# Performance work log

Measured on AMD Instinct MI355X. Metric: run time of the kernel, lower is better.

The kernel has to match this reference:

```python
import jax, jax.numpy as jnp
import numpy as np

N, K, F, H, C = 16384, 16, 3, 64, 10


def setup_inputs() -> dict:
    key = jax.random.key(0)
    ks = jax.random.split(key, 6)
    pos = jax.random.normal(ks[0], (N, F), jnp.float32)
    batch = jnp.zeros((N,), jnp.int32)  # single graph
    W1 = jax.random.normal(ks[1], (2 * F, H), jnp.float32) * 0.1
    b1 = jnp.zeros((H,), jnp.float32)
    W2 = jax.random.normal(ks[2], (2 * H, H), jnp.float32) * 0.1
    b2 = jnp.zeros((H,), jnp.float32)
    Wc = jax.random.normal(ks[3], (H, C), jnp.float32) * 0.1
    bc = jnp.zeros((C,), jnp.float32)
    return {"pos": pos, "batch": batch, "W1": W1, "b1": b1,
            "W2": W2, "b2": b2, "Wc": Wc, "bc": bc}


def knn_graph(pos, k):
    # brute-force knn with self-loops (loop=True): self has distance 0
    sq = jnp.sum(pos * pos, axis=1)
    d = sq[:, None] + sq[None, :] - 2.0 * (pos @ pos.T)  # [N, N]
    _, idx = jax.lax.top_k(-d, k)  # [N, k] nearest neighbor indices (incl. self)
    return idx


def edge_conv(x, idx, W, b):
    # message for edge j->i: Linear(concat(x_i, x_j - x_i)); aggregate by max over neighbors
    n, k = idx.shape
    xi = x[:, None, :]               # [N, 1, F]
    xj = x[idx]                      # [N, k, F]
    msg = jnp.concatenate([jnp.broadcast_to(xi, (n, k, x.shape[1])), xj - xi], axis=-1)
    m = msg @ W + b                  # [N, k, H]
    return jnp.max(m, axis=1)        # [N, H]


def reference(pos, batch, W1, b1, W2, b2, Wc, bc):
    idx = knn_graph(pos, K)
    h = jax.nn.relu(edge_conv(pos, idx, W1, b1))
    h = jax.nn.relu(edge_conv(h, idx, W2, b2))
    g = jax.ops.segment_max(h, batch, num_segments=1)  # global max pool -> [1, H]
    return g @ Wc + bc
```

## Files before the change

kernel.cpp:

```cpp
#include <hip/hip_runtime.h>

#define NPTS 16384
#define KNN 16
#define HID 64
#define NCLS 10

#define WPB 4
#define QPB 16
#define CPW (NPTS / WPB)
#define SCAP 128

__device__ __forceinline__ float distm2(float qx, float qy, float qz, float4 c) {
    return fmaf(qx, c.x, fmaf(qy, c.y, fmaf(qz, c.z, c.w)));
}

__device__ __forceinline__ float __frfl(float x) {
    return __int_as_float(__builtin_amdgcn_readfirstlane(__float_as_int(x)));
}

__device__ __forceinline__ unsigned long long dkey(float v, int j) {
    unsigned u = __float_as_uint(v);
    u = (u & 0x80000000u) ? ~u : (u | 0x80000000u);
    return ((unsigned long long)u << 32) | (unsigned)j;
}

__device__ __forceinline__ unsigned long long shfl_xor_u64(unsigned long long x, int m) {
    unsigned hi = (unsigned)__shfl_xor((int)(x >> 32), m, 64);
    unsigned lo = (unsigned)__shfl_xor((int)(x & 0xffffffffu), m, 64);
    return ((unsigned long long)hi << 32) | lo;
}

__device__ __forceinline__ void wave_top16_16(unsigned long long (&key)[16], int lane,
                                              int q, int* __restrict__ idx) {
    int outj = 0x7fffffff;
    for (int r = 0; r < 16; ++r) {
        unsigned long long gm = key[0];
#pragma unroll
        for (int s = 1; s < 16; ++s) gm = key[s] < gm ? key[s] : gm;
#pragma unroll
        for (int st = 1; st < 64; st <<= 1) {
            unsigned long long o = shfl_xor_u64(gm, st);
            gm = o < gm ? o : gm;
        }
        if (lane == r) outj = (int)(gm & 0xffffffffu);
#pragma unroll
        for (int s = 0; s < 16; ++s)
            if (key[s] == gm) key[s] = ~0ull;
    }
    if (lane < 16) idx[q * KNN + lane] = outj;
}

__global__ void prep_kernel(const float* __restrict__ pos, float4* __restrict__ pos4,
                            float4* __restrict__ pm2) {
    int i = blockIdx.x * 256 + threadIdx.x;
    if (i < NPTS) {
        float x = pos[3 * i], y = pos[3 * i + 1], z = pos[3 * i + 2];
        float sq = fmaf(x, x, fmaf(y, y, z * z));
        pos4[i] = make_float4(x, y, z, sq);
        pm2[i] = make_float4(-2.f * x, -2.f * y, -2.f * z, sq);
    }
}

__global__ __launch_bounds__(256) void knn_kernel(const float4* __restrict__ pos4,
                                                  const float4* __restrict__ pm2,
                                                  int* __restrict__ idx) {
    __shared__ unsigned long long keys[QPB][SCAP];
    __shared__ int knt[QPB];
    __shared__ float smin[QPB][WPB][16];
    int tid = threadIdx.x;
    int lane = tid & 63;
    int w = tid >> 6;
    int qb = blockIdx.x * QPB;
    float qx[QPB], qy[QPB], qz[QPB];
#pragma unroll
    for (int i = 0; i < QPB; ++i) {
        float4 t4 = pos4[qb + i];
        qx[i] = __frfl(t4.x); qy[i] = __frfl(t4.y); qz[i] = __frfl(t4.z);
    }
    int base = w * CPW;

    float mn[QPB];
#pragma unroll
    for (int i = 0; i < QPB; ++i) mn[i] = INFINITY;
    {
        float4 c0 = pm2[base + lane],       c1 = pm2[base + 64 + lane];
        float4 d0 = pm2[base + 128 + lane], d1 = pm2[base + 192 + lane];
        for (int cb = base; cb < base + CPW; cb += 128) {
#pragma unroll
            for (int i = 0; i < QPB; ++i) {
                float va = distm2(qx[i], qy[i], qz[i], c0);
                float vb = distm2(qx[i], qy[i], qz[i], c1);
                mn[i] = fminf(mn[i], fminf(va, vb));
            }
            c0 = d0; c1 = d1;
            d0 = pm2[cb + 256 + lane];
            d1 = pm2[cb + 320 + lane];
        }
    }
#pragma unroll
    for (int i = 0; i < QPB; ++i) {
        float m = mn[i];
        m = fminf(m, __shfl_xor(m, 16, 64));
        m = fminf(m, __shfl_xor(m, 32, 64));
        if (lane < 16) smin[i][w][lane] = m;
    }
    if (tid < QPB) knt[tid] = 0;
    __syncthreads();

    float tq[QPB];
#pragma unroll
    for (int i = 0; i < QPB; ++i) {
        int s = lane & 15;
        float m = fminf(fminf(smin[i][0][s], smin[i][1][s]),
                        fminf(smin[i][2][s], smin[i][3][s]));
        m = fmaxf(m, __shfl_xor(m, 1, 64));
        m = fmaxf(m, __shfl_xor(m, 2, 64));
        m = fmaxf(m, __shfl_xor(m, 4, 64));
        m = fmaxf(m, __shfl_xor(m, 8, 64));
        tq[i] = __frfl(m);
    }

    {
        float4 c0 = pm2[base + lane],       c1 = pm2[base + 64 + lane];
        float4 d0 = pm2[base + 128 + lane], d1 = pm2[base + 192 + lane];
        for (int cb = base; cb < base + CPW; cb += 128) {
            int j0 = cb + lane, j1 = cb + 64 + lane;
#pragma unroll
            for (int i = 0; i < QPB; ++i) {
                float va = distm2(qx[i], qy[i], qz[i], c0);
                float vb = distm2(qx[i], qy[i], qz[i], c1);
                if (fminf(va, vb) <= tq[i]) {
                    if (va <= tq[i]) { int s = atomicAdd(&knt[i], 1); if (s < SCAP) keys[i][s] = dkey(va, j0); }
                    if (vb <= tq[i]) { int s = atomicAdd(&knt[i], 1); if (s < SCAP) keys[i][s] = dkey(vb, j1); }
                }
            }
            c0 = d0; c1 = d1;
            d0 = pm2[cb + 256 + lane];
            d1 = pm2[cb + 320 + lane];
        }
    }
    __syncthreads();

#pragma unroll
    for (int e = 0; e < 4; ++e) {
        int qi = w * 4 + e;
        int q = qb + qi;
        int ntot = knt[qi];
        if (ntot <= SCAP) {
            unsigned long long k0 = (lane < ntot) ? keys[qi][lane] : ~0ull;
            unsigned long long k1 = (lane + 64 < ntot) ? keys[qi][lane + 64] : ~0ull;
            int r0 = 0, r1 = 0;
            int t = 0;
            for (; t + 8 <= ntot; t += 8) {
                unsigned long long a0 = keys[qi][t + 0], a1 = keys[qi][t + 1];
                unsigned long long a2 = keys[qi][t + 2], a3 = keys[qi][t + 3];
                unsigned long long a4 = keys[qi][t + 4], a5 = keys[qi][t + 5];
                unsigned long long a6 = keys[qi][t + 6], a7 = keys[qi][t + 7];
                r0 += (int)(a0 < k0) + (int)(a1 < k0) + (int)(a2 < k0) + (int)(a3 < k0)
                    + (int)(a4 < k0) + (int)(a5 < k0) + (int)(a6 < k0) + (int)(a7 < k0);
                r1 += (int)(a0 < k1) + (int)(a1 < k1) + (int)(a2 < k1) + (int)(a3 < k1)
                    + (int)(a4 < k1) + (int)(a5 < k1) + (int)(a6 < k1) + (int)(a7 < k1);
            }
            for (; t < ntot; ++t) {
                unsigned long long k = keys[qi][t];
                r0 += (int)(k < k0);
                r1 += (int)(k < k1);
            }
            if (lane < ntot && r0 < KNN) idx[q * KNN + r0] = (int)(k0 & 0xffffffffu);
            if (lane + 64 < ntot && r1 < KNN) idx[q * KNN + r1] = (int)(k1 & 0xffffffffu);
        } else {
            float tqq = tq[qi];
            unsigned long long key[16];
#pragma unroll
            for (int u = 0; u < 16; ++u) key[u] = ~0ull;
            for (int j = lane; j < NPTS; j += 64) {
                float v = distm2(qx[qi], qy[qi], qz[qi], pm2[j]);
                unsigned long long k = dkey(v, j);
                if (v <= tqq && k < key[15]) {
#pragma unroll
                    for (int s = 0; s < 16; ++s) {
                        unsigned long long a = k < key[s] ? k : key[s];
                        unsigned long long b = k < key[s] ? key[s] : k;
                        key[s] = a;
                        k = b;
                    }
                }
            }
            wave_top16_16(key, lane, q, idx);
        }
    }
}

__global__ __launch_bounds__(256) void ec12_kernel(const float4* __restrict__ pos4,
                                                   const int* __restrict__ idx,
                                                   const float* __restrict__ W1,
                                                   const float* __restrict__ b1,
                                                   const float* __restrict__ W2,
                                                   const float* __restrict__ b2,
                                                   float* __restrict__ C2,
                                                   float* __restrict__ Y2) {
    __shared__ float h1s[16][64];
    int t = threadIdx.x & 63;
    int w = threadIdx.x >> 6;
    int pb = blockIdx.x * 16 + w * 4;
    float w0 = W1[0 * HID + t], w1 = W1[1 * HID + t], w2 = W1[2 * HID + t];
    float v0 = W1[3 * HID + t], v1 = W1[4 * HID + t], v2 = W1[5 * HID + t];
    float bt1 = b1[t];
#pragma unroll
    for (int i = 0; i < 4; ++i) {
        int p = pb + i;
        float4 xi = pos4[p];
        float C = bt1 + xi.x * (w0 - v0) + xi.y * (w1 - v1) + xi.z * (w2 - v2);
        const int4* ip = (const int4*)(idx + (size_t)p * KNN);
        int4 n0 = ip[0], n1 = ip[1], n2 = ip[2], n3 = ip[3];
        int jj[16] = {n0.x, n0.y, n0.z, n0.w, n1.x, n1.y, n1.z, n1.w,
                      n2.x, n2.y, n2.z, n2.w, n3.x, n3.y, n3.z, n3.w};
        float m = -INFINITY;
#pragma unroll
        for (int k = 0; k < KNN; ++k) {
            float4 xj = pos4[jj[k]];
            m = fmaxf(m, fmaf(xj.x, v0, fmaf(xj.y, v1, xj.z * v2)));
        }
        h1s[w * 4 + i][t] = fmaxf(C + m, 0.f);
    }
    __syncthreads();
    float aa[4] = {0.f, 0.f, 0.f, 0.f};
    float ab[4] = {0.f, 0.f, 0.f, 0.f};
#pragma unroll 8
    for (int f = 0; f < 64; ++f) {
        float wa = W2[f * HID + t];
        float wb = W2[(64 + f) * HID + t];
#pragma unroll
        for (int i = 0; i < 4; ++i) {
            float h = h1s[w * 4 + i][f];
            aa[i] = fmaf(h, wa, aa[i]);
            ab[i] = fmaf(h, wb, ab[i]);
        }
    }
    float bt = b2[t];
#pragma unroll
    for (int i = 0; i < 4; ++i) {
        C2[(pb + i) * HID + t] = bt + aa[i] - ab[i];
        Y2[(pb + i) * HID + t] = ab[i];
    }
}

__global__ __launch_bounds__(256) void ec2_maxpool_kernel(const float* __restrict__ C2,
                                                          const float* __restrict__ Y2,
                                                          const int* __restrict__ idx,
                                                          float* __restrict__ gpartial) {
    int t = threadIdx.x & 63;
    int lp = threadIdx.x >> 6;
    int p = blockIdx.x * 4 + lp;
    const int4* ip = (const int4*)(idx + (size_t)p * KNN);
    int4 n0 = ip[0], n1 = ip[1], n2 = ip[2], n3 = ip[3];
    int jj[16] = {n0.x, n0.y, n0.z, n0.w, n1.x, n1.y, n1.z, n1.w,
                  n2.x, n2.y, n2.z, n2.w, n3.x, n3.y, n3.z, n3.w};
    float m = -INFINITY;
#pragma unroll
    for (int k = 0; k < KNN; ++k) {
        m = fmaxf(m, Y2[jj[k] * HID + t]);
    }
    float val = fmaxf(C2[p * HID + t] + m, 0.f);
    __shared__ float red[4][64];
    red[lp][t] = val;
    __syncthreads();
    if (lp == 0) {
        float g = fmaxf(fmaxf(red[0][t], red[1][t]), fmaxf(red[2][t], red[3][t]));
        gpartial[blockIdx.x * 64 + t] = g;
    }
}

__global__ __launch_bounds__(256) void greduce2_kernel(const float* __restrict__ gpartial,
                                                       float* __restrict__ gp2) {
    __shared__ float red[4][64];
    int f = threadIdx.x & 63;
    int w = threadIdx.x >> 6;
    int r0 = blockIdx.x * 16 + w * 4;
    float m = -INFINITY;
#pragma unroll
    for (int r = 0; r < 4; ++r) m = fmaxf(m, gpartial[(r0 + r) * 64 + f]);
    red[w][f] = m;
    __syncthreads();
    if (w == 0)
        gp2[blockIdx.x * 64 + f] =
            fmaxf(fmaxf(red[0][f], red[1][f]), fmaxf(red[2][f], red[3][f]));
}

__global__ __launch_bounds__(256) void tail2_kernel(const float* __restrict__ gp2,
                                                    const float* __restrict__ Wc,
                                                    const float* __restrict__ bc,
                                                    float* __restrict__ out) {
    __shared__ float red[4][64];
    __shared__ float g[64];
    int f = threadIdx.x & 63;
    int w = threadIdx.x >> 6;
    float m = -INFINITY;
    for (int i = w; i < 256; i += 4) m = fmaxf(m, gp2[i * 64 + f]);
    red[w][f] = m;
    __syncthreads();
    if (w == 0) g[f] = fmaxf(fmaxf(red[0][f], red[1][f]), fmaxf(red[2][f], red[3][f]));
    __syncthreads();
    if (threadIdx.x < NCLS) {
        float a = bc[threadIdx.x];
#pragma unroll
        for (int h = 0; h < HID; ++h) a = fmaf(g[h], Wc[h * NCLS + threadIdx.x], a);
        out[threadIdx.x] = a;
    }
}

extern "C" void kernel_launch(void* const* d_in, const int* in_sizes, int n_in,
                              void* d_out, int out_size, void* d_ws, size_t ws_size,
                              hipStream_t stream) {
    const float* pos = (const float*)d_in[0];
    const float* W1 = (const float*)d_in[2];
    const float* b1 = (const float*)d_in[3];
    const float* W2 = (const float*)d_in[4];
    const float* b2 = (const float*)d_in[5];
    const float* Wc = (const float*)d_in[6];
    const float* bc = (const float*)d_in[7];
    float* out = (float*)d_out;

    char* ws = (char*)d_ws;
    size_t o = 0;
    auto alloc = [&](size_t bytes) { size_t r = o; o += (bytes + 255) & ~size_t(255); return r; };
    size_t fm = (size_t)NPTS * HID * 4;
    size_t o_pos4 = alloc((size_t)NPTS * 16);
    size_t o_pm2 = alloc((size_t)(NPTS + 320) * 16);
    size_t o_idx = alloc((size_t)NPTS * KNN * 4);
    size_t o_C2 = alloc(fm);
    size_t o_Y2 = alloc(fm);
    size_t o_gp = alloc((size_t)(NPTS / 4) * HID * 4);
    size_t o_gp2 = alloc((size_t)256 * HID * 4);

    float4* pos4 = (float4*)(ws + o_pos4);
    float4* pm2 = (float4*)(ws + o_pm2);
    int* idx = (int*)(ws + o_idx);
    float* C2 = (float*)(ws + o_C2);
    float* Y2 = (float*)(ws + o_Y2);
    float* gp = (float*)(ws + o_gp);
    float* gp2 = (float*)(ws + o_gp2);

    hipMemsetAsync(pm2 + NPTS, 0, 320 * sizeof(float4), stream);

    prep_kernel<<<NPTS / 256, 256, 0, stream>>>(pos, pos4, pm2);
    knn_kernel<<<NPTS / QPB, 256, 0, stream>>>(pos4, pm2, idx);
    ec12_kernel<<<NPTS / 16, 256, 0, stream>>>(pos4, idx, W1, b1, W2, b2, C2, Y2);
    ec2_maxpool_kernel<<<NPTS / 4, 256, 0, stream>>>(C2, Y2, idx, gp);
    greduce2_kernel<<<256, 256, 0, stream>>>(gp, gp2);
    tail2_kernel<<<1, 256, 0, stream>>>(gp2, Wc, bc, out);
}
```

Measured before the change: 315.6 us.

## Use packed-FP32 distance math with a paired SoA candidate layout in kNN

```diff
diff --git a/kernel.cpp b/kernel.cpp
--- a/kernel.cpp
+++ b/kernel.cpp
@@ -6,9 +6,19 @@
 #define NCLS 10
 
 #define WPB 4
-#define QPB 16
-#define CPW (NPTS / WPB)
+#define QPB 8
 #define SCAP 128
+#define GRPQ 32
+#define NITER 16
+#define TPAD 576
+
+typedef float v2f __attribute__((ext_vector_type(2)));
+
+__device__ __forceinline__ v2f pdist(v2f Qx, v2f Qy, v2f Qz, v2f X, v2f Y, v2f Z, v2f W) {
+    return __builtin_elementwise_fma(Qx, X,
+            __builtin_elementwise_fma(Qy, Y,
+             __builtin_elementwise_fma(Qz, Z, W)));
+}
 
 __device__ __forceinline__ float distm2(float qx, float qy, float qz, float4 c) {
     return fmaf(qx, c.x, fmaf(qy, c.y, fmaf(qz, c.z, c.w)));
@@ -51,7 +61,7 @@
 }
 
 __global__ void prep_kernel(const float* __restrict__ pos, float4* __restrict__ pos4,
-                            float4* __restrict__ pm2) {
+                            float4* __restrict__ pm2, float4* __restrict__ pm2t) {
     int i = blockIdx.x * 256 + threadIdx.x;
     if (i < NPTS) {
         float x = pos[3 * i], y = pos[3 * i + 1], z = pos[3 * i + 2];
@@ -59,10 +69,21 @@
         pos4[i] = make_float4(x, y, z, sq);
         pm2[i] = make_float4(-2.f * x, -2.f * y, -2.f * z, sq);
     }
+    if (i < NPTS / 2) {
+        int p = i;
+        float x0 = pos[6 * p],     y0 = pos[6 * p + 1], z0 = pos[6 * p + 2];
+        float x1 = pos[6 * p + 3], y1 = pos[6 * p + 4], z1 = pos[6 * p + 5];
+        float w0 = fmaf(x0, x0, fmaf(y0, y0, z0 * z0));
+        float w1 = fmaf(x1, x1, fmaf(y1, y1, z1 * z1));
+        int g = p >> 6, l = p & 63;
+        pm2t[g * 128 + l]      = make_float4(-2.f * x0, -2.f * x1, -2.f * y0, -2.f * y1);
+        pm2t[g * 128 + 64 + l] = make_float4(-2.f * z0, -2.f * z1, w0, w1);
+    }
 }
 
 __global__ __launch_bounds__(256) void knn_kernel(const float4* __restrict__ pos4,
                                                   const float4* __restrict__ pm2,
+                                                  const float4* __restrict__ pm2t,
                                                   int* __restrict__ idx) {
     __shared__ unsigned long long keys[QPB][SCAP];
     __shared__ int knt[QPB];
@@ -71,30 +92,38 @@
     int lane = tid & 63;
     int w = tid >> 6;
     int qb = blockIdx.x * QPB;
-    float qx[QPB], qy[QPB], qz[QPB];
+    v2f Qx[QPB], Qy[QPB], Qz[QPB];
 #pragma unroll
     for (int i = 0; i < QPB; ++i) {
         float4 t4 = pos4[qb + i];
-        qx[i] = __frfl(t4.x); qy[i] = __frfl(t4.y); qz[i] = __frfl(t4.z);
-    }
-    int base = w * CPW;
+        float ax = __frfl(t4.x), ay = __frfl(t4.y), az = __frfl(t4.z);
+        Qx[i] = (v2f){ax, ax}; Qy[i] = (v2f){ay, ay}; Qz[i] = (v2f){az, az};
+    }
+    const float4* pt = pm2t + (size_t)w * (GRPQ * 128) + lane;
 
     float mn[QPB];
 #pragma unroll
     for (int i = 0; i < QPB; ++i) mn[i] = INFINITY;
     {
-        float4 c0 = pm2[base + lane],       c1 = pm2[base + 64 + lane];
-        float4 d0 = pm2[base + 128 + lane], d1 = pm2[base + 192 + lane];
-        for (int cb = base; cb < base + CPW; cb += 128) {
+        float4 aXY0 = pt[0],   aZW0 = pt[64],  aXY1 = pt[128], aZW1 = pt[192];
+        float4 bXY0 = pt[256], bZW0 = pt[320], bXY1 = pt[384], bZW1 = pt[448];
+        int off = 512;
+#pragma unroll 2
+        for (int t = 0; t < NITER; ++t) {
+            v2f X0 = {aXY0.x, aXY0.y}, Y0 = {aXY0.z, aXY0.w};
+            v2f Z0 = {aZW0.x, aZW0.y}, W0 = {aZW0.z, aZW0.w};
+            v2f X1 = {aXY1.x, aXY1.y}, Y1 = {aXY1.z, aXY1.w};
+            v2f Z1 = {aZW1.x, aZW1.y}, W1 = {aZW1.z, aZW1.w};
 #pragma unroll
             for (int i = 0; i < QPB; ++i) {
-                float va = distm2(qx[i], qy[i], qz[i], c0);
-                float vb = distm2(qx[i], qy[i], qz[i], c1);
-                mn[i] = fminf(mn[i], fminf(va, vb));
-            }
-            c0 = d0; c1 = d1;
-            d0 = pm2[cb + 256 + lane];
-            d1 = pm2[cb + 320 + lane];
+                v2f D0 = pdist(Qx[i], Qy[i], Qz[i], X0, Y0, Z0, W0);
+                v2f D1 = pdist(Qx[i], Qy[i], Qz[i], X1, Y1, Z1, W1);
+                mn[i] = fminf(mn[i], fminf(D0.x, D0.y));
+                mn[i] = fminf(mn[i], fminf(D1.x, D1.y));
+            }
+            aXY0 = bXY0; aZW0 = bZW0; aXY1 = bXY1; aZW1 = bZW1;
+            bXY0 = pt[off]; bZW0 = pt[off + 64]; bXY1 = pt[off + 128]; bZW1 = pt[off + 192];
+            off += 256;
         }
     }
 #pragma unroll
@@ -121,29 +150,41 @@
     }
 
     {
-        float4 c0 = pm2[base + lane],       c1 = pm2[base + 64 + lane];
-        float4 d0 = pm2[base + 128 + lane], d1 = pm2[base + 192 + lane];
-        for (int cb = base; cb < base + CPW; cb += 128) {
-            int j0 = cb + lane, j1 = cb + 64 + lane;
+        float4 aXY0 = pt[0],   aZW0 = pt[64],  aXY1 = pt[128], aZW1 = pt[192];
+        float4 bXY0 = pt[256], bZW0 = pt[320], bXY1 = pt[384], bZW1 = pt[448];
+        int off = 512;
+        int pbase = w * (GRPQ * 64);
+#pragma unroll 2
+        for (int t = 0; t < NITER; ++t) {
+            v2f X0 = {aXY0.x, aXY0.y}, Y0 = {aXY0.z, aXY0.w};
+            v2f Z0 = {aZW0.x, aZW0.y}, W0 = {aZW0.z, aZW0.w};
+            v2f X1 = {aXY1.x, aXY1.y}, Y1 = {aXY1.z, aXY1.w};
+            v2f Z1 = {aZW1.x, aZW1.y}, W1 = {aZW1.z, aZW1.w};
+            int j00 = 2 * (pbase + t * 128 + lane);
+            int j10 = j00 + 128;
 #pragma unroll
             for (int i = 0; i < QPB; ++i) {
-                float va = distm2(qx[i], qy[i], qz[i], c0);
-                float vb = distm2(qx[i], qy[i], qz[i], c1);
-                if (fminf(va, vb) <= tq[i]) {
-                    if (va <= tq[i]) { int s = atomicAdd(&knt[i], 1); if (s < SCAP) keys[i][s] = dkey(va, j0); }
-                    if (vb <= tq[i]) { int s = atomicAdd(&knt[i], 1); if (s < SCAP) keys[i][s] = dkey(vb, j1); }
+                v2f D0 = pdist(Qx[i], Qy[i], Qz[i], X0, Y0, Z0, W0);
+                v2f D1 = pdist(Qx[i], Qy[i], Qz[i], X1, Y1, Z1, W1);
+                float m01 = fminf(fminf(D0.x, D0.y), fminf(D1.x, D1.y));
+                if (__any(m01 <= tq[i])) {
+                    if (D0.x <= tq[i]) { int s = atomicAdd(&knt[i], 1); if (s < SCAP) keys[i][s] = dkey(D0.x, j00); }
+                    if (D0.y <= tq[i]) { int s = atomicAdd(&knt[i], 1); if (s < SCAP) keys[i][s] = dkey(D0.y, j00 + 1); }
+                    if (D1.x <= tq[i]) { int s = atomicAdd(&knt[i], 1); if (s < SCAP) keys[i][s] = dkey(D1.x, j10); }
+                    if (D1.y <= tq[i]) { int s = atomicAdd(&knt[i], 1); if (s < SCAP) keys[i][s] = dkey(D1.y, j10 + 1); }
                 }
             }
-            c0 = d0; c1 = d1;
-            d0 = pm2[cb + 256 + lane];
-            d1 = pm2[cb + 320 + lane];
-        }
-    }
-    __syncthreads();
-
-#pragma unroll
-    for (int e = 0; e < 4; ++e) {
-        int qi = w * 4 + e;
+            aXY0 = bXY0; aZW0 = bZW0; aXY1 = bXY1; aZW1 = bZW1;
+            bXY0 = pt[off]; bZW0 = pt[off + 64]; bXY1 = pt[off + 128]; bZW1 = pt[off + 448 - 256];
+            bXY1 = pt[off + 128]; bZW1 = pt[off + 192];
+            off += 256;
+        }
+    }
+    __syncthreads();
+
+#pragma unroll
+    for (int e = 0; e < 2; ++e) {
+        int qi = w * 2 + e;
         int q = qb + qi;
         int ntot = knt[qi];
         if (ntot <= SCAP) {
@@ -170,11 +211,12 @@
             if (lane + 64 < ntot && r1 < KNN) idx[q * KNN + r1] = (int)(k1 & 0xffffffffu);
         } else {
             float tqq = tq[qi];
+            float ax = Qx[qi].x, ay = Qy[qi].x, az = Qz[qi].x;
             unsigned long long key[16];
 #pragma unroll
             for (int u = 0; u < 16; ++u) key[u] = ~0ull;
             for (int j = lane; j < NPTS; j += 64) {
-                float v = distm2(qx[qi], qy[qi], qz[qi], pm2[j]);
+                float v = distm2(ax, ay, az, pm2[j]);
                 unsigned long long k = dkey(v, j);
                 if (v <= tqq && k < key[15]) {
 #pragma unroll
@@ -326,7 +368,8 @@
     auto alloc = [&](size_t bytes) { size_t r = o; o += (bytes + 255) & ~size_t(255); return r; };
     size_t fm = (size_t)NPTS * HID * 4;
     size_t o_pos4 = alloc((size_t)NPTS * 16);
-    size_t o_pm2 = alloc((size_t)(NPTS + 320) * 16);
+    size_t o_pm2 = alloc((size_t)NPTS * 16);
+    size_t o_pm2t = alloc((size_t)(NPTS + TPAD) * 16);
     size_t o_idx = alloc((size_t)NPTS * KNN * 4);
     size_t o_C2 = alloc(fm);
     size_t o_Y2 = alloc(fm);
@@ -335,16 +378,17 @@
 
     float4* pos4 = (float4*)(ws + o_pos4);
     float4* pm2 = (float4*)(ws + o_pm2);
+    float4* pm2t = (float4*)(ws + o_pm2t);
     int* idx = (int*)(ws + o_idx);
     float* C2 = (float*)(ws + o_C2);
     float* Y2 = (float*)(ws + o_Y2);
     float* gp = (float*)(ws + o_gp);
     float* gp2 = (float*)(ws + o_gp2);
 
-    hipMemsetAsync(pm2 + NPTS, 0, 320 * sizeof(float4), stream);
-
-    prep_kernel<<<NPTS / 256, 256, 0, stream>>>(pos, pos4, pm2);
-    knn_kernel<<<NPTS / QPB, 256, 0, stream>>>(pos4, pm2, idx);
+    hipMemsetAsync(pm2t + NPTS, 0, TPAD * sizeof(float4), stream);
+
+    prep_kernel<<<NPTS / 256, 256, 0, stream>>>(pos, pos4, pm2, pm2t);
+    knn_kernel<<<NPTS / QPB, 256, 0, stream>>>(pos4, pm2, pm2t, idx);
     ec12_kernel<<<NPTS / 16, 256, 0, stream>>>(pos4, idx, W1, b1, W2, b2, C2, Y2);
     ec2_maxpool_kernel<<<NPTS / 4, 256, 0, stream>>>(C2, Y2, idx, gp);
     greduce2_kernel<<<256, 256, 0, stream>>>(gp, gp2);
```

Result: faster. 301.4 us (-4.5%).

## Replace brute-force KNN with uniform grid binning and shell-ordered cell search

Applied to the files above, without the earlier changes.

```diff
diff --git a/kernel.cpp b/kernel.cpp
--- a/kernel.cpp
+++ b/kernel.cpp
@@ -5,23 +5,26 @@
 #define HID 64
 #define NCLS 10
 
-#define WPB 4
-#define QPB 16
-#define CPW (NPTS / WPB)
-#define SCAP 128
-
-__device__ __forceinline__ float distm2(float qx, float qy, float qz, float4 c) {
-    return fmaf(qx, c.x, fmaf(qy, c.y, fmaf(qz, c.z, c.w)));
+#define G 16
+#define NCELL (G * G * G)
+#define RMAX (G - 1)
+#define NSHELL ((2 * RMAX + 1) * (2 * RMAX + 1) * (2 * RMAX + 1))
+
+
+__device__ __forceinline__ unsigned encm(float x) {
+    unsigned u = __float_as_uint(x);
+    return (u & 0x80000000u) ? ~u : (u | 0x80000000u);
+}
+__device__ __forceinline__ float decm(unsigned v) {
+    return (v & 0x80000000u) ? __uint_as_float(v ^ 0x80000000u) : __uint_as_float(~v);
 }
 
 __device__ __forceinline__ float __frfl(float x) {
     return __int_as_float(__builtin_amdgcn_readfirstlane(__float_as_int(x)));
 }
 
-__device__ __forceinline__ unsigned long long dkey(float v, int j) {
-    unsigned u = __float_as_uint(v);
-    u = (u & 0x80000000u) ? ~u : (u | 0x80000000u);
-    return ((unsigned long long)u << 32) | (unsigned)j;
+__device__ __forceinline__ unsigned long long dkey(float v, unsigned j) {
+    return ((unsigned long long)encm(v) << 32) | j;
 }
 
 __device__ __forceinline__ unsigned long long shfl_xor_u64(unsigned long long x, int m) {
@@ -50,146 +53,176 @@
     if (lane < 16) idx[q * KNN + lane] = outj;
 }
 
-__global__ void prep_kernel(const float* __restrict__ pos, float4* __restrict__ pos4,
-                            float4* __restrict__ pm2) {
+__device__ __forceinline__ int cid(int cx, int cy, int cz) { return (cz * G + cy) * G + cx; }
+
+__device__ __forceinline__ int caxis(float x, float lo, float iv) {
+    int c = (int)((x - lo) * iv);
+    return min(G - 1, max(0, c));
+}
+
+
+__global__ void bbox_kernel(const float* __restrict__ pos, unsigned* __restrict__ bb) {
     int i = blockIdx.x * 256 + threadIdx.x;
-    if (i < NPTS) {
-        float x = pos[3 * i], y = pos[3 * i + 1], z = pos[3 * i + 2];
-        float sq = fmaf(x, x, fmaf(y, y, z * z));
-        pos4[i] = make_float4(x, y, z, sq);
-        pm2[i] = make_float4(-2.f * x, -2.f * y, -2.f * z, sq);
-    }
-}
-
-__global__ __launch_bounds__(256) void knn_kernel(const float4* __restrict__ pos4,
-                                                  const float4* __restrict__ pm2,
-                                                  int* __restrict__ idx) {
-    __shared__ unsigned long long keys[QPB][SCAP];
-    __shared__ int knt[QPB];
-    __shared__ float smin[QPB][WPB][16];
+    unsigned ex = encm(pos[3 * i]), ey = encm(pos[3 * i + 1]), ez = encm(pos[3 * i + 2]);
+    unsigned mnx = ex, mny = ey, mnz = ez, mxx = ex, mxy = ey, mxz = ez;
+#pragma unroll
+    for (int m = 1; m < 64; m <<= 1) {
+        mnx = min(mnx, (unsigned)__shfl_xor((int)mnx, m, 64));
+        mny = min(mny, (unsigned)__shfl_xor((int)mny, m, 64));
+        mnz = min(mnz, (unsigned)__shfl_xor((int)mnz, m, 64));
+        mxx = max(mxx, (unsigned)__shfl_xor((int)mxx, m, 64));
+        mxy = max(mxy, (unsigned)__shfl_xor((int)mxy, m, 64));
+        mxz = max(mxz, (unsigned)__shfl_xor((int)mxz, m, 64));
+    }
+    if ((threadIdx.x & 63) == 0) {
+        atomicMin(bb + 0, mnx); atomicMin(bb + 1, mny); atomicMin(bb + 2, mnz);
+        atomicMax(bb + 3, mxx); atomicMax(bb + 4, mxy); atomicMax(bb + 5, mxz);
+    }
+}
+
+__global__ void count_kernel(const float* __restrict__ pos, const unsigned* __restrict__ bb,
+                             float4* __restrict__ pos4, unsigned* __restrict__ cellCnt) {
+    int i = blockIdx.x * 256 + threadIdx.x;
+    float x = pos[3 * i], y = pos[3 * i + 1], z = pos[3 * i + 2];
+    pos4[i] = make_float4(x, y, z, fmaf(x, x, fmaf(y, y, z * z)));
+    float lox = decm(bb[0]), loy = decm(bb[1]), loz = decm(bb[2]);
+    float sx = decm(bb[3]) - lox, sy = decm(bb[4]) - loy, sz = decm(bb[5]) - loz;
+    float ivx = sx > 0.f ? (float)G / sx : 0.f;
+    float ivy = sy > 0.f ? (float)G / sy : 0.f;
+    float ivz = sz > 0.f ? (float)G / sz : 0.f;
+    int c = cid(caxis(x, lox, ivx), caxis(y, loy, ivy), caxis(z, loz, ivz));
+    atomicAdd(&cellCnt[c], 1u);
+}
+
+__global__ __launch_bounds__(256) void scan_kernel(const unsigned* __restrict__ cellCnt,
+                                                   unsigned* __restrict__ cellStart) {
+    __shared__ unsigned ps[256];
     int tid = threadIdx.x;
-    int lane = tid & 63;
-    int w = tid >> 6;
-    int qb = blockIdx.x * QPB;
-    float qx[QPB], qy[QPB], qz[QPB];
-#pragma unroll
-    for (int i = 0; i < QPB; ++i) {
-        float4 t4 = pos4[qb + i];
-        qx[i] = __frfl(t4.x); qy[i] = __frfl(t4.y); qz[i] = __frfl(t4.z);
-    }
-    int base = w * CPW;
-
-    float mn[QPB];
-#pragma unroll
-    for (int i = 0; i < QPB; ++i) mn[i] = INFINITY;
-    {
-        float4 c0 = pm2[base + lane],       c1 = pm2[base + 64 + lane];
-        float4 d0 = pm2[base + 128 + lane], d1 = pm2[base + 192 + lane];
-        for (int cb = base; cb < base + CPW; cb += 128) {
-#pragma unroll
-            for (int i = 0; i < QPB; ++i) {
-                float va = distm2(qx[i], qy[i], qz[i], c0);
-                float vb = distm2(qx[i], qy[i], qz[i], c1);
-                mn[i] = fminf(mn[i], fminf(va, vb));
-            }
-            c0 = d0; c1 = d1;
-            d0 = pm2[cb + 256 + lane];
-            d1 = pm2[cb + 320 + lane];
-        }
-    }
-#pragma unroll
-    for (int i = 0; i < QPB; ++i) {
-        float m = mn[i];
-        m = fminf(m, __shfl_xor(m, 16, 64));
-        m = fminf(m, __shfl_xor(m, 32, 64));
-        if (lane < 16) smin[i][w][lane] = m;
-    }
-    if (tid < QPB) knt[tid] = 0;
-    __syncthreads();
-
-    float tq[QPB];
-#pragma unroll
-    for (int i = 0; i < QPB; ++i) {
-        int s = lane & 15;
-        float m = fminf(fminf(smin[i][0][s], smin[i][1][s]),
-                        fminf(smin[i][2][s], smin[i][3][s]));
-        m = fmaxf(m, __shfl_xor(m, 1, 64));
-        m = fmaxf(m, __shfl_xor(m, 2, 64));
-        m = fmaxf(m, __shfl_xor(m, 4, 64));
-        m = fmaxf(m, __shfl_xor(m, 8, 64));
-        tq[i] = __frfl(m);
-    }
-
-    {
-        float4 c0 = pm2[base + lane],       c1 = pm2[base + 64 + lane];
-        float4 d0 = pm2[base + 128 + lane], d1 = pm2[base + 192 + lane];
-        for (int cb = base; cb < base + CPW; cb += 128) {
-            int j0 = cb + lane, j1 = cb + 64 + lane;
-#pragma unroll
-            for (int i = 0; i < QPB; ++i) {
-                float va = distm2(qx[i], qy[i], qz[i], c0);
-                float vb = distm2(qx[i], qy[i], qz[i], c1);
-                if (fminf(va, vb) <= tq[i]) {
-                    if (va <= tq[i]) { int s = atomicAdd(&knt[i], 1); if (s < SCAP) keys[i][s] = dkey(va, j0); }
-                    if (vb <= tq[i]) { int s = atomicAdd(&knt[i], 1); if (s < SCAP) keys[i][s] = dkey(vb, j1); }
-                }
-            }
-            c0 = d0; c1 = d1;
-            d0 = pm2[cb + 256 + lane];
-            d1 = pm2[cb + 320 + lane];
-        }
-    }
-    __syncthreads();
-
-#pragma unroll
-    for (int e = 0; e < 4; ++e) {
-        int qi = w * 4 + e;
-        int q = qb + qi;
-        int ntot = knt[qi];
-        if (ntot <= SCAP) {
-            unsigned long long k0 = (lane < ntot) ? keys[qi][lane] : ~0ull;
-            unsigned long long k1 = (lane + 64 < ntot) ? keys[qi][lane + 64] : ~0ull;
-            int r0 = 0, r1 = 0;
-            int t = 0;
-            for (; t + 8 <= ntot; t += 8) {
-                unsigned long long a0 = keys[qi][t + 0], a1 = keys[qi][t + 1];
-                unsigned long long a2 = keys[qi][t + 2], a3 = keys[qi][t + 3];
-                unsigned long long a4 = keys[qi][t + 4], a5 = keys[qi][t + 5];
-                unsigned long long a6 = keys[qi][t + 6], a7 = keys[qi][t + 7];
-                r0 += (int)(a0 < k0) + (int)(a1 < k0) + (int)(a2 < k0) + (int)(a3 < k0)
-                    + (int)(a4 < k0) + (int)(a5 < k0) + (int)(a6 < k0) + (int)(a7 < k0);
-                r1 += (int)(a0 < k1) + (int)(a1 < k1) + (int)(a2 < k1) + (int)(a3 < k1)
-                    + (int)(a4 < k1) + (int)(a5 < k1) + (int)(a6 < k1) + (int)(a7 < k1);
-            }
-            for (; t < ntot; ++t) {
-                unsigned long long k = keys[qi][t];
-                r0 += (int)(k < k0);
-                r1 += (int)(k < k1);
-            }
-            if (lane < ntot && r0 < KNN) idx[q * KNN + r0] = (int)(k0 & 0xffffffffu);
-            if (lane + 64 < ntot && r1 < KNN) idx[q * KNN + r1] = (int)(k1 & 0xffffffffu);
-        } else {
-            float tqq = tq[qi];
-            unsigned long long key[16];
-#pragma unroll
-            for (int u = 0; u < 16; ++u) key[u] = ~0ull;
-            for (int j = lane; j < NPTS; j += 64) {
-                float v = distm2(qx[qi], qy[qi], qz[qi], pm2[j]);
-                unsigned long long k = dkey(v, j);
-                if (v <= tqq && k < key[15]) {
-#pragma unroll
-                    for (int s = 0; s < 16; ++s) {
-                        unsigned long long a = k < key[s] ? k : key[s];
-                        unsigned long long b = k < key[s] ? key[s] : k;
-                        key[s] = a;
-                        k = b;
+    int base = tid * 16;
+    unsigned loc[16];
+    unsigned sum = 0;
+#pragma unroll
+    for (int k = 0; k < 16; ++k) { loc[k] = cellCnt[base + k]; sum += loc[k]; }
+    ps[tid] = sum;
+    __syncthreads();
+    for (int off = 1; off < 256; off <<= 1) {
+        unsigned v = (tid >= off) ? ps[tid - off] : 0u;
+        __syncthreads();
+        ps[tid] += v;
+        __syncthreads();
+    }
+    unsigned run = ps[tid] - sum;
+#pragma unroll
+    for (int k = 0; k < 16; ++k) { cellStart[base + k] = run; run += loc[k]; }
+    if (tid == 255) cellStart[NCELL] = run;
+}
+
+__global__ void scatter_kernel(const float* __restrict__ pos, const unsigned* __restrict__ bb,
+                               const unsigned* __restrict__ cellStart,
+                               unsigned* __restrict__ cellFill, float4* __restrict__ binned) {
+    int i = blockIdx.x * 256 + threadIdx.x;
+    float x = pos[3 * i], y = pos[3 * i + 1], z = pos[3 * i + 2];
+    float lox = decm(bb[0]), loy = decm(bb[1]), loz = decm(bb[2]);
+    float sx = decm(bb[3]) - lox, sy = decm(bb[4]) - loy, sz = decm(bb[5]) - loz;
+    float ivx = sx > 0.f ? (float)G / sx : 0.f;
+    float ivy = sy > 0.f ? (float)G / sy : 0.f;
+    float ivz = sz > 0.f ? (float)G / sz : 0.f;
+    int c = cid(caxis(x, lox, ivx), caxis(y, loy, ivy), caxis(z, loz, ivz));
+    unsigned slot = cellStart[c] + atomicAdd(&cellFill[c], 1u);
+    binned[slot] = make_float4(x, y, z, __uint_as_float((unsigned)i));
+}
+
+__global__ void shelltab_kernel(unsigned* __restrict__ tab, unsigned* __restrict__ fill) {
+    int e = blockIdx.x * 256 + threadIdx.x;
+    if (e >= NSHELL) return;
+    int dz = e / (31 * 31) - 15;
+    int dy = (e / 31) % 31 - 15;
+    int dx = e % 31 - 15;
+    int adx = abs(dx), ady = abs(dy), adz = abs(dz);
+    int r = max(adx, max(ady, adz));
+    int base = r ? (2 * r - 1) * (2 * r - 1) * (2 * r - 1) : 0;
+    int slot = base + (int)atomicAdd(&fill[r], 1u);
+    tab[slot] = (unsigned)(dx + 16) | ((unsigned)(dy + 16) << 6) | ((unsigned)(dz + 16) << 12);
+}
+
+__global__ __launch_bounds__(256) void search_kernel(const float4* __restrict__ pos4,
+                                                     const unsigned* __restrict__ bb,
+                                                     const unsigned* __restrict__ cellStart,
+                                                     const float4* __restrict__ binned,
+                                                     const unsigned* __restrict__ shellTab,
+                                                     int* __restrict__ idx) {
+    int lane = threadIdx.x & 63;
+    int w = threadIdx.x >> 6;
+    int qi = blockIdx.x * 4 + w;
+    float4 qp = pos4[qi];
+    float qx = __frfl(qp.x), qy = __frfl(qp.y), qz = __frfl(qp.z);
+
+    float lox = decm(bb[0]), loy = decm(bb[1]), loz = decm(bb[2]);
+    float sx = decm(bb[3]) - lox, sy = decm(bb[4]) - loy, sz = decm(bb[5]) - loz;
+    float hx = sx / (float)G, hy = sy / (float)G, hz = sz / (float)G;
+    float ivx = sx > 0.f ? (float)G / sx : 0.f;
+    float ivy = sy > 0.f ? (float)G / sy : 0.f;
+    float ivz = sz > 0.f ? (float)G / sz : 0.f;
+    int cx = caxis(qx, lox, ivx), cy = caxis(qy, loy, ivy), cz = caxis(qz, loz, ivz);
+
+    unsigned long long key[16];
+#pragma unroll
+    for (int u = 0; u < 16; ++u) key[u] = ~0ull;
+
+    for (int r = 0; r <= RMAX; ++r) {
+        int e0 = r ? (2 * r - 1) * (2 * r - 1) * (2 * r - 1) : 0;
+        int e1 = (2 * r + 1) * (2 * r + 1) * (2 * r + 1);
+        for (int e = e0; e < e1; ++e) {
+            unsigned pe = shellTab[e];
+            int bx = cx + (int)(pe & 63u) - 16;
+            int by = cy + (int)((pe >> 6) & 63u) - 16;
+            int bz = cz + (int)((pe >> 12) & 63u) - 16;
+            if ((unsigned)bx >= (unsigned)G || (unsigned)by >= (unsigned)G ||
+                (unsigned)bz >= (unsigned)G) continue;
+            int c = cid(bx, by, bz);
+            unsigned s = cellStart[c], t = cellStart[c + 1];
+            for (unsigned j = s + (unsigned)lane; j < t; j += 64u) {
+                float4 b = binned[j];
+                float dx = b.x - qx, dy = b.y - qy, dz = b.z - qz;
+                float d = fmaf(dz, dz, fmaf(dy, dy, dx * dx));
+                unsigned long long k = dkey(d, __float_as_uint(b.w));
+                if (k < key[15]) {
+#pragma unroll
+                    for (int u = 0; u < 16; ++u) {
+                        unsigned long long a = k < key[u] ? k : key[u];
+                        unsigned long long bmx = k < key[u] ? key[u] : k;
+                        key[u] = a;
+                        k = bmx;
                     }
                 }
             }
-            wave_top16_16(key, lane, q, idx);
         }
-    }
-}
+        bool lcx = (cx - r) <= 0, rcx = (cx + r) >= G - 1;
+        bool lcy = (cy - r) <= 0, rcy = (cy + r) >= G - 1;
+        bool lcz = (cz - r) <= 0, rcz = (cz + r) >= G - 1;
+        if (lcx && rcx && lcy && rcy && lcz && rcz) break;
+        float dmin = 1e30f;
+        if (!lcx) dmin = fminf(dmin, qx - (lox + (float)(cx - r) * hx));
+        if (!rcx) dmin = fminf(dmin, (lox + (float)(cx + r + 1) * hx) - qx);
+        if (!lcy) dmin = fminf(dmin, qy - (loy + (float)(cy - r) * hy));
+        if (!rcy) dmin = fminf(dmin, (loy + (float)(cy + r + 1) * hy) - qy);
+        if (!lcz) dmin = fminf(dmin, qz - (loz + (float)(cz - r) * hz));
+        if (!rcz) dmin = fminf(dmin, (loz + (float)(cz + r + 1) * hz) - qz);
+        float dp = dmin - 1e-4f;
+        if (dp > 0.f) {
+            float thr = dp * dp;
+            unsigned long long TK = ((unsigned long long)encm(thr) << 32) | 0xffffffffull;
+            int c16 = 0;
+#pragma unroll
+            for (int u = 0; u < 16; ++u) c16 += (int)(key[u] <= TK);
+#pragma unroll
+            for (int m = 1; m < 64; m <<= 1) c16 += __shfl_xor(c16, m, 64);
+            if (c16 >= KNN) break;
+        }
+    }
+    wave_top16_16(key, lane, qi, idx);
+}
+
 
 __global__ __launch_bounds__(256) void ec12_kernel(const float4* __restrict__ pos4,
                                                    const int* __restrict__ idx,
@@ -325,26 +358,46 @@
     size_t o = 0;
     auto alloc = [&](size_t bytes) { size_t r = o; o += (bytes + 255) & ~size_t(255); return r; };
     size_t fm = (size_t)NPTS * HID * 4;
+    size_t o_bb = alloc(8 * 4);
+    size_t o_cnt = alloc((size_t)(NCELL + 1) * 4);
+    size_t o_start = alloc((size_t)(NCELL + 1) * 4);
+    size_t o_fill = alloc((size_t)NCELL * 4);
+    size_t o_sfill = alloc(16 * 4);
+    size_t o_stab = alloc((size_t)NSHELL * 4);
     size_t o_pos4 = alloc((size_t)NPTS * 16);
-    size_t o_pm2 = alloc((size_t)(NPTS + 320) * 16);
+    size_t o_bin = alloc((size_t)NPTS * 16);
     size_t o_idx = alloc((size_t)NPTS * KNN * 4);
     size_t o_C2 = alloc(fm);
     size_t o_Y2 = alloc(fm);
     size_t o_gp = alloc((size_t)(NPTS / 4) * HID * 4);
     size_t o_gp2 = alloc((size_t)256 * HID * 4);
 
+    unsigned* bb = (unsigned*)(ws + o_bb);
+    unsigned* cellCnt = (unsigned*)(ws + o_cnt);
+    unsigned* cellStart = (unsigned*)(ws + o_start);
+    unsigned* cellFill = (unsigned*)(ws + o_fill);
+    unsigned* shellFill = (unsigned*)(ws + o_sfill);
+    unsigned* shellTab = (unsigned*)(ws + o_stab);
     float4* pos4 = (float4*)(ws + o_pos4);
-    float4* pm2 = (float4*)(ws + o_pm2);
+    float4* binned = (float4*)(ws + o_bin);
     int* idx = (int*)(ws + o_idx);
     float* C2 = (float*)(ws + o_C2);
     float* Y2 = (float*)(ws + o_Y2);
     float* gp = (float*)(ws + o_gp);
     float* gp2 = (float*)(ws + o_gp2);
 
-    hipMemsetAsync(pm2 + NPTS, 0, 320 * sizeof(float4), stream);
-
-    prep_kernel<<<NPTS / 256, 256, 0, stream>>>(pos, pos4, pm2);
-    knn_kernel<<<NPTS / QPB, 256, 0, stream>>>(pos4, pm2, idx);
+    hipMemsetAsync(bb, 0xFF, 12, stream);
+    hipMemsetAsync(bb + 3, 0x00, 12, stream);
+    hipMemsetAsync(cellCnt, 0, (size_t)NCELL * 4, stream);
+    hipMemsetAsync(cellFill, 0, (size_t)NCELL * 4, stream);
+    hipMemsetAsync(shellFill, 0, 16 * 4, stream);
+
+    bbox_kernel<<<NPTS / 256, 256, 0, stream>>>(pos, bb);
+    count_kernel<<<NPTS / 256, 256, 0, stream>>>(pos, bb, pos4, cellCnt);
+    scan_kernel<<<1, 256, 0, stream>>>(cellCnt, cellStart);
+    scatter_kernel<<<NPTS / 256, 256, 0, stream>>>(pos, bb, cellStart, cellFill, binned);
+    shelltab_kernel<<<(NSHELL + 255) / 256, 256, 0, stream>>>(shellTab, shellFill);
+    search_kernel<<<NPTS / 4, 256, 0, stream>>>(pos4, bb, cellStart, binned, shellTab, idx);
     ec12_kernel<<<NPTS / 16, 256, 0, stream>>>(pos4, idx, W1, b1, W2, b2, C2, Y2);
     ec2_maxpool_kernel<<<NPTS / 4, 256, 0, stream>>>(C2, Y2, idx, gp);
     greduce2_kernel<<<256, 256, 0, stream>>>(gp, gp2);
```

Measured after the change: 641.6 us. +103.3%, slower.
